# Kernel optimization log

Measured on AMD Instinct MI355X. Metric: run time of the kernel, lower is better.

The kernel has to match this reference:

```python
import jax, jax.numpy as jnp
import numpy as np

B, S, D, H, F, E = 4, 1024, 1024, 16, 4096, 8
HD = D // H  # head dim


def setup_inputs() -> dict:
    key = jax.random.key(0)
    ks = jax.random.split(key, 8)
    p = lambda k, shp: jax.random.normal(k, shp, jnp.float32) * 0.02
    return {
        "x": jax.random.normal(ks[0], (B, S, D), jnp.float32),
        "mask": jnp.ones((B, S), jnp.int32),
        "in_proj_w": p(ks[1], (3 * D, D)),
        "in_proj_b": jnp.zeros((3 * D,), jnp.float32),
        "out_proj_w": p(ks[2], (D, D)),
        "out_proj_b": jnp.zeros((D,), jnp.float32),
        "ln1_g": jnp.ones((D,), jnp.float32),
        "ln1_b": jnp.zeros((D,), jnp.float32),
        "ln2_g": jnp.ones((D,), jnp.float32),
        "ln2_b": jnp.zeros((D,), jnp.float32),
        "gate_w": p(ks[3], (E, D)),
        "gate_b": jnp.zeros((E,), jnp.float32),
        "w1": p(ks[4], (E, F, D)),
        "b1": jnp.zeros((E, F), jnp.float32),
        "w2": p(ks[5], (E, D, F)),
        "b2": jnp.zeros((E, D), jnp.float32),
    }


def _layernorm(x, g, b, eps=1e-5):
    m = x.mean(-1, keepdims=True)
    v = ((x - m) ** 2).mean(-1, keepdims=True)
    return (x - m) / jnp.sqrt(v + eps) * g + b


def _mha(x, key_pad, in_proj_w, in_proj_b, out_proj_w, out_proj_b):
    # combined QKV projection as in torch nn.MultiheadAttention
    qkv = x @ in_proj_w.T + in_proj_b  # (B,S,3D)
    q, k, v = jnp.split(qkv, 3, axis=-1)
    def heads(t):
        return t.reshape(B, S, H, HD).transpose(0, 2, 1, 3)  # (B,H,S,HD)
    q, k, v = heads(q), heads(k), heads(v)
    scores = jnp.einsum("bhqd,bhkd->bhqk", q, k) / jnp.sqrt(jnp.float32(HD))
    scores = jnp.where(key_pad[:, None, None, :], -1e30, scores)
    attn = jax.nn.softmax(scores, axis=-1)
    out = jnp.einsum("bhqk,bhkd->bhqd", attn, v)  # (B,H,S,HD)
    out = out.transpose(0, 2, 1, 3).reshape(B, S, D)
    return out @ out_proj_w.T + out_proj_b


def _moe(x, gate_w, gate_b, w1, b1, w2, b2):
    logits = x @ gate_w.T + gate_b            # (B,S,E)
    probs = jax.nn.softmax(logits, axis=-1)
    # dense all-expert FFN (faithful to original: every expert computed)
    h = jax.nn.relu(jnp.einsum("bsd,efd->bsef", x, w1) + b1)   # (B,S,E,F)
    all_out = jnp.einsum("bsef,edf->bsed", h, w2) + b2          # (B,S,E,D)
    top_vals, top_idx = jax.lax.top_k(probs, 2)                 # (B,S,2)
    weights = top_vals / (top_vals.sum(-1, keepdims=True) + 1e-9)
    sel = jnp.take_along_axis(all_out, top_idx[..., None], axis=2)  # (B,S,2,D)
    return (sel * weights[..., None]).sum(axis=2)


def reference(x, mask, in_proj_w, in_proj_b, out_proj_w, out_proj_b,
              ln1_g, ln1_b, ln2_g, ln2_b, gate_w, gate_b, w1, b1, w2, b2):
    key_pad = mask == 0  # (B,S) bool
    attn_out = _mha(x, key_pad, in_proj_w, in_proj_b, out_proj_w, out_proj_b)
    x1 = _layernorm(x + attn_out, ln1_g, ln1_b)
    ff = _moe(x1, gate_w, gate_b, w1, b1, w2, b2)
    return _layernorm(x1 + ff, ln2_g, ln2_b)
```

## Files before the change

### kernel.cpp

```cpp
#include <hip/hip_runtime.h>

typedef __attribute__((ext_vector_type(8))) short bf16x8;
typedef __attribute__((ext_vector_type(4))) float f32x4;

#define DEV __device__ __forceinline__

static constexpr int Bb = 4, Sq = 1024, Dd = 1024, Hh = 16, HDd = 64, Ff = 4096, Ee = 8;
static constexpr int Nn = Bb * Sq;
static constexpr int TD = 3 * Dd;
static constexpr int PMAX = 2 * Nn + Ee * 128;

DEV unsigned short f2bf(float x) {
  union { float f; unsigned u; } c; c.f = x;
  unsigned r = c.u + 0x7FFFu + ((c.u >> 16) & 1u);
  return (unsigned short)(r >> 16);
}

typedef const __attribute__((address_space(1))) unsigned int* gas_t;
typedef __attribute__((address_space(3))) unsigned int* las_t;
DEV void gload16(const void* g, void* l) {
  __builtin_amdgcn_global_load_lds((gas_t)g, (las_t)l, 16, 0, 0);
}

__global__ __launch_bounds__(256) void cvt_kernel(const float* __restrict__ in,
                                                  unsigned short* __restrict__ out) {
  int i = blockIdx.x * 256 + threadIdx.x;
  const float4 a = *(const float4*)(in + (size_t)i * 8);
  const float4 b = *(const float4*)(in + (size_t)i * 8 + 4);
  union { uint4 u; unsigned short s[8]; } pk;
  pk.s[0] = f2bf(a.x); pk.s[1] = f2bf(a.y); pk.s[2] = f2bf(a.z); pk.s[3] = f2bf(a.w);
  pk.s[4] = f2bf(b.x); pk.s[5] = f2bf(b.y); pk.s[6] = f2bf(b.z); pk.s[7] = f2bf(b.w);
  *(uint4*)(out + (size_t)i * 8) = pk.u;
}

template <int EPI>
__global__ __launch_bounds__(256) void gemm_bt(
    const unsigned short* __restrict__ A, const unsigned short* __restrict__ Bw,
    const float* __restrict__ bias, void* __restrict__ o0, void* __restrict__ o1,
    void* __restrict__ o2, int M, int Ncols, int K,
    const int* __restrict__ poff) {
  int bx, by;
  {
    const int gx = gridDim.x, nwg = gx * gridDim.y;
    int orig = blockIdx.y * gx + blockIdx.x;
    int q = nwg >> 3, r = nwg & 7;
    int xcd = orig & 7, lin = orig >> 3;
    int wg = (xcd < r ? xcd * (q + 1) : r * (q + 1) + (xcd - r) * q) + lin;
    bx = wg % gx; by = wg / gx;
  }
  const int m0 = bx * 128;
  int e = 0;
  if constexpr (EPI >= 2) {
    if (m0 >= poff[Ee]) return;
#pragma unroll
    for (int k = 1; k < Ee; ++k) if (m0 >= poff[k]) e = k;
  } else {
    if (m0 >= M) return;
  }
  const int n0 = by * 128;
  const unsigned short* Bptr = Bw + (size_t)e * Ncols * K;
  const float* biasptr = bias + e * Ncols;

  __shared__ __align__(128) unsigned short As[128 * 64];
  __shared__ __align__(128) unsigned short Bs[128 * 64];

  const int tid = threadIdx.x;
  const int lane = tid & 63, wid = tid >> 6;
  const int wm = wid >> 1, wn = wid & 1;
  const int lr = lane & 15, lk = lane >> 4;

  const char* aSrc[4]; const char* bSrc[4];
  char* aDst[4]; char* bDst[4];
#pragma unroll
  for (int it = 0; it < 4; ++it) {
    int b = it * 4096 + tid * 16;
    int r = b >> 7;
    int colb = (b & 127) ^ ((r & 7) << 4);
    aSrc[it] = (const char*)(A + (size_t)(m0 + r) * K) + colb;
    bSrc[it] = (const char*)(Bptr + (size_t)(n0 + r) * K) + colb;
    aDst[it] = (char*)As + it * 4096 + wid * 1024;
    bDst[it] = (char*)Bs + it * 4096 + wid * 1024;
  }
  int aOff[2][4], bOff[2][4];
#pragma unroll
  for (int ks = 0; ks < 2; ++ks)
#pragma unroll
    for (int i = 0; i < 4; ++i) {
      int ra = wm * 64 + i * 16 + lr;
      aOff[ks][i] = ra * 64 + (((ks * 4 + lk) ^ (ra & 7)) << 3);
      int rb = wn * 64 + i * 16 + lr;
      bOff[ks][i] = rb * 64 + (((ks * 4 + lk) ^ (rb & 7)) << 3);
    }

  f32x4 acc[4][4] = {};

  for (int k0 = 0; k0 < K; k0 += 64) {
#pragma unroll
    for (int it = 0; it < 4; ++it) gload16(aSrc[it] + (size_t)k0 * 2, aDst[it]);
#pragma unroll
    for (int it = 0; it < 4; ++it) gload16(bSrc[it] + (size_t)k0 * 2, bDst[it]);
    __syncthreads();
#pragma unroll
    for (int ks = 0; ks < 2; ++ks) {
      bf16x8 af[4], bfv[4];
#pragma unroll
      for (int mi = 0; mi < 4; ++mi) af[mi] = *(const bf16x8*)&As[aOff[ks][mi]];
#pragma unroll
      for (int ni = 0; ni < 4; ++ni) bfv[ni] = *(const bf16x8*)&Bs[bOff[ks][ni]];
#pragma unroll
      for (int mi = 0; mi < 4; ++mi)
#pragma unroll
        for (int ni = 0; ni < 4; ++ni)
          acc[mi][ni] = __builtin_amdgcn_mfma_f32_16x16x32_bf16(af[mi], bfv[ni], acc[mi][ni], 0, 0, 0);
    }
    __syncthreads();
  }

#pragma unroll
  for (int ni = 0; ni < 4; ++ni) {
    const int col = n0 + wn * 64 + ni * 16 + lr;
    const float bv = biasptr[col];
#pragma unroll
    for (int mi = 0; mi < 4; ++mi) {
#pragma unroll
      for (int i = 0; i < 4; ++i) {
        const int mloc = wm * 64 + mi * 16 + lk * 4 + i;
        float v = acc[mi][ni][i] + bv;
        if constexpr (EPI == 0) {
          int t = m0 + mloc;
          int which = col >> 10, jj = col & 1023, hh = jj >> 6, hd = jj & 63;
          int bb = t >> 10, s = t & 1023;
          unsigned short* dst = (which == 0) ? (unsigned short*)o0
                              : (which == 1) ? (unsigned short*)o1 : (unsigned short*)o2;
          dst[((size_t)(bb * Hh + hh) * Sq + s) * HDd + hd] = f2bf(v);
        } else if constexpr (EPI == 1) {
          ((float*)o0)[(size_t)(m0 + mloc) * Dd + col] = v;
        } else if constexpr (EPI == 2) {
          ((unsigned short*)o0)[(size_t)(m0 + mloc) * Ff + col] = f2bf(fmaxf(v, 0.f));
        } else {
          ((float*)o0)[(size_t)(m0 + mloc) * Dd + col] = v;
        }
      }
    }
  }
}

__global__ __launch_bounds__(256) void attn_kernel(
    const unsigned short* __restrict__ qb, const unsigned short* __restrict__ kb,
    const unsigned short* __restrict__ vb, const int* __restrict__ mask,
    unsigned short* __restrict__ attnb) {
  const int qt = blockIdx.x, h = blockIdx.y, b = blockIdx.z;
  const unsigned short* Q = qb + (size_t)(b * Hh + h) * Sq * HDd;
  const unsigned short* Kg = kb + (size_t)(b * Hh + h) * Sq * HDd;
  const unsigned short* Vg = vb + (size_t)(b * Hh + h) * Sq * HDd;

  __shared__ unsigned short Qs[64 * 72], Ks[64 * 72], Vt[64 * 72], Ps[64 * 72];
  __shared__ float Ssm[64 * 65];
  __shared__ float mS[64], lS[64], aS[64];
  __shared__ int mk[64];

  const int tid = threadIdx.x, lane = tid & 63, wid = tid >> 6;
  const int lr = lane & 15, lk = lane >> 4;

#pragma unroll
  for (int it = 0; it < 2; ++it) {
    int c = tid + it * 256; int r = c >> 3, kc = (c & 7) * 8;
    *(uint4*)&Qs[r * 72 + kc] = *(const uint4*)(Q + (size_t)(qt * 64 + r) * 64 + kc);
  }
  if (tid < 64) { mS[tid] = -1e30f; lS[tid] = 0.f; }

  f32x4 oacc[4] = {};

  for (int kt = 0; kt < 16; ++kt) {
    __syncthreads();
#pragma unroll
    for (int it = 0; it < 2; ++it) {
      int c = tid + it * 256; int r = c >> 3, kc = (c & 7) * 8;
      *(uint4*)&Ks[r * 72 + kc] = *(const uint4*)(Kg + (size_t)(kt * 64 + r) * 64 + kc);
    }
    {
      int kk = tid >> 2, hg = (tid & 3) * 16;
      union { uint4 u[2]; unsigned short s[16]; } tv;
      tv.u[0] = *(const uint4*)(Vg + (size_t)(kt * 64 + kk) * 64 + hg);
      tv.u[1] = *(const uint4*)(Vg + (size_t)(kt * 64 + kk) * 64 + hg + 8);
#pragma unroll
      for (int j = 0; j < 16; ++j) Vt[(hg + j) * 72 + kk] = tv.s[j];
    }
    if (tid < 64) mk[tid] = mask[b * Sq + kt * 64 + tid];
    __syncthreads();

    f32x4 sacc[4] = {};
#pragma unroll
    for (int ks = 0; ks < 2; ++ks) {
      bf16x8 aq = *(const bf16x8*)&Qs[(wid * 16 + lr) * 72 + ks * 32 + lk * 8];
#pragma unroll
      for (int ni = 0; ni < 4; ++ni) {
        bf16x8 bk = *(const bf16x8*)&Ks[(ni * 16 + lr) * 72 + ks * 32 + lk * 8];
        sacc[ni] = __builtin_amdgcn_mfma_f32_16x16x32_bf16(aq, bk, sacc[ni], 0, 0, 0);
      }
    }
#pragma unroll
    for (int ni = 0; ni < 4; ++ni)
#pragma unroll
      for (int i = 0; i < 4; ++i) {
        int r = wid * 16 + lk * 4 + i, cc = ni * 16 + lr;
        float v = sacc[ni][i] * 0.125f;
        if (mk[cc] == 0) v = -1e30f;
        Ssm[r * 65 + cc] = v;
      }
    __syncthreads();
    {
      int r = tid >> 2, cg = (tid & 3) * 16;
      float xv[16];
#pragma unroll
      for (int j = 0; j < 16; ++j) xv[j] = Ssm[r * 65 + cg + j];
      float mx = xv[0];
#pragma unroll
      for (int j = 1; j < 16; ++j) mx = fmaxf(mx, xv[j]);
      mx = fmaxf(mx, __shfl_xor(mx, 1));
      mx = fmaxf(mx, __shfl_xor(mx, 2));
      float mprev = mS[r];
      float mnew = fmaxf(mprev, mx);
      float sum = 0.f;
      union { uint4 u[2]; unsigned short s[16]; } pb;
#pragma unroll
      for (int j = 0; j < 16; ++j) {
        float pv = expf(xv[j] - mnew);
        sum += pv; pb.s[j] = f2bf(pv);
      }
      sum += __shfl_xor(sum, 1);
      sum += __shfl_xor(sum, 2);
      *(uint4*)&Ps[r * 72 + cg] = pb.u[0];
      *(uint4*)&Ps[r * 72 + cg + 8] = pb.u[1];
      if ((tid & 3) == 0) {
        float alpha = expf(mprev - mnew);
        mS[r] = mnew; aS[r] = alpha; lS[r] = lS[r] * alpha + sum;
      }
    }
    __syncthreads();
#pragma unroll
    for (int ni = 0; ni < 4; ++ni)
#pragma unroll
      for (int i = 0; i < 4; ++i)
        oacc[ni][i] *= aS[wid * 16 + lk * 4 + i];
#pragma unroll
    for (int ks = 0; ks < 2; ++ks) {
      bf16x8 ap = *(const bf16x8*)&Ps[(wid * 16 + lr) * 72 + ks * 32 + lk * 8];
#pragma unroll
      for (int ni = 0; ni < 4; ++ni) {
        bf16x8 bv = *(const bf16x8*)&Vt[(ni * 16 + lr) * 72 + ks * 32 + lk * 8];
        oacc[ni] = __builtin_amdgcn_mfma_f32_16x16x32_bf16(ap, bv, oacc[ni], 0, 0, 0);
      }
    }
  }
  __syncthreads();
#pragma unroll
  for (int ni = 0; ni < 4; ++ni)
#pragma unroll
    for (int i = 0; i < 4; ++i) {
      int r = wid * 16 + lk * 4 + i;
      int q = qt * 64 + r;
      float v = oacc[ni][i] / lS[r];
      attnb[((size_t)(b * Sq + q)) * Dd + h * 64 + ni * 16 + lr] = f2bf(v);
    }
}

__global__ __launch_bounds__(256) void ln_kernel(
    const float* __restrict__ a, const float* __restrict__ b2,
    const float* __restrict__ g, const float* __restrict__ beta,
    float* __restrict__ outf, unsigned short* __restrict__ outb) {
  const int t = blockIdx.x, tid = threadIdx.x;
  float4 v = *(const float4*)(a + (size_t)t * Dd + tid * 4);
  {
    float4 u = *(const float4*)(b2 + (size_t)t * Dd + tid * 4);
    v.x += u.x; v.y += u.y; v.z += u.z; v.w += u.w;
  }
  const int lane = tid & 63, wid = tid >> 6;
  float s = v.x + v.y + v.z + v.w;
  for (int sh = 1; sh < 64; sh <<= 1) s += __shfl_xor(s, sh);
  __shared__ float red[4], red2[4];
  if (lane == 0) red[wid] = s;
  __syncthreads();
  float mean = (red[0] + red[1] + red[2] + red[3]) * (1.f / Dd);
  float dx = v.x - mean, dy = v.y - mean, dz = v.z - mean, dw = v.w - mean;
  float q = dx * dx + dy * dy + dz * dz + dw * dw;
  for (int sh = 1; sh < 64; sh <<= 1) q += __shfl_xor(q, sh);
  if (lane == 0) red2[wid] = q;
  __syncthreads();
  float var = (red2[0] + red2[1] + red2[2] + red2[3]) * (1.f / Dd);
  float rstd = rsqrtf(var + 1e-5f);
  float4 gg = *(const float4*)(g + tid * 4);
  float4 bb = *(const float4*)(beta + tid * 4);
  float4 o;
  o.x = dx * rstd * gg.x + bb.x;
  o.y = dy * rstd * gg.y + bb.y;
  o.z = dz * rstd * gg.z + bb.z;
  o.w = dw * rstd * gg.w + bb.w;
  if (outf) *(float4*)(outf + (size_t)t * Dd + tid * 4) = o;
  if (outb) {
    ushort4 pk; pk.x = f2bf(o.x); pk.y = f2bf(o.y); pk.z = f2bf(o.z); pk.w = f2bf(o.w);
    *(ushort4*)(outb + (size_t)t * Dd + tid * 4) = pk;
  }
}

__global__ __launch_bounds__(256) void ln2_kernel(
    const float* __restrict__ x1f, const float* __restrict__ ffp,
    const int* __restrict__ inv, const float* __restrict__ wtok,
    const float* __restrict__ g, const float* __restrict__ beta,
    float* __restrict__ out) {
  const int t = blockIdx.x, tid = threadIdx.x;
  const int i0 = inv[2 * t], i1 = inv[2 * t + 1];
  const float w0 = wtok[2 * t], w1 = wtok[2 * t + 1];
  float4 v = *(const float4*)(x1f + (size_t)t * Dd + tid * 4);
  float4 u0 = *(const float4*)(ffp + (size_t)i0 * Dd + tid * 4);
  float4 u1 = *(const float4*)(ffp + (size_t)i1 * Dd + tid * 4);
  v.x += w0 * u0.x + w1 * u1.x; v.y += w0 * u0.y + w1 * u1.y;
  v.z += w0 * u0.z + w1 * u1.z; v.w += w0 * u0.w + w1 * u1.w;
  const int lane = tid & 63, wid = tid >> 6;
  float s = v.x + v.y + v.z + v.w;
  for (int sh = 1; sh < 64; sh <<= 1) s += __shfl_xor(s, sh);
  __shared__ float red[4], red2[4];
  if (lane == 0) red[wid] = s;
  __syncthreads();
  float mean = (red[0] + red[1] + red[2] + red[3]) * (1.f / Dd);
  float dx = v.x - mean, dy = v.y - mean, dz = v.z - mean, dw = v.w - mean;
  float q = dx * dx + dy * dy + dz * dz + dw * dw;
  for (int sh = 1; sh < 64; sh <<= 1) q += __shfl_xor(q, sh);
  if (lane == 0) red2[wid] = q;
  __syncthreads();
  float var = (red2[0] + red2[1] + red2[2] + red2[3]) * (1.f / Dd);
  float rstd = rsqrtf(var + 1e-5f);
  float4 gg = *(const float4*)(g + tid * 4);
  float4 bb = *(const float4*)(beta + tid * 4);
  float4 o;
  o.x = dx * rstd * gg.x + bb.x;
  o.y = dy * rstd * gg.y + bb.y;
  o.z = dz * rstd * gg.z + bb.z;
  o.w = dw * rstd * gg.w + bb.w;
  *(float4*)(out + (size_t)t * Dd + tid * 4) = o;
}

__global__ __launch_bounds__(256) void route_kernel(
    const float* __restrict__ x1f, const float* __restrict__ gw, const float* __restrict__ gb,
    int* __restrict__ cnt, int* __restrict__ tokslot, float* __restrict__ wtok) {
  __shared__ float gws[Ee * Dd];
  const int tid = threadIdx.x;
#pragma unroll
  for (int it = 0; it < 8; ++it) {
    int idx = (tid + it * 256) * 4;
    *(float4*)&gws[idx] = *(const float4*)(gw + idx);
  }
  __syncthreads();
  const int lane = tid & 63, wid = tid >> 6;
  for (int it = 0; it < 16; ++it) {
    int t = blockIdx.x * 64 + wid * 16 + it;
    float acc[Ee] = {};
    for (int i = 0; i < 16; ++i) {
      float xv = x1f[(size_t)t * Dd + i * 64 + lane];
#pragma unroll
      for (int e = 0; e < Ee; ++e) acc[e] += xv * gws[e * Dd + i * 64 + lane];
    }
#pragma unroll
    for (int e = 0; e < Ee; ++e) {
      float vv = acc[e];
      for (int sh = 1; sh < 64; sh <<= 1) vv += __shfl_xor(vv, sh);
      acc[e] = vv;
    }
    if (lane == 0) {
      float lg[Ee];
#pragma unroll
      for (int e = 0; e < Ee; ++e) lg[e] = acc[e] + gb[e];
      float m = lg[0];
#pragma unroll
      for (int e = 1; e < Ee; ++e) m = fmaxf(m, lg[e]);
      float p[Ee], ssum = 0.f;
#pragma unroll
      for (int e = 0; e < Ee; ++e) { p[e] = expf(lg[e] - m); ssum += p[e]; }
      int e0 = 0;
#pragma unroll
      for (int e = 1; e < Ee; ++e) if (p[e] > p[e0]) e0 = e;
      int e1 = -1;
#pragma unroll
      for (int e = 0; e < Ee; ++e) {
        if (e == e0) continue;
        if (e1 < 0 || p[e] > p[e1]) e1 = e;
      }
      float v0 = p[e0] / ssum, v1 = p[e1] / ssum;
      float wsum = v0 + v1 + 1e-9f;
      wtok[t * 2] = v0 / wsum; wtok[t * 2 + 1] = v1 / wsum;
      int p0 = atomicAdd(&cnt[e0], 1);
      tokslot[e0 * Nn + p0] = t * 2;
      int p1 = atomicAdd(&cnt[e1], 1);
      tokslot[e1 * Nn + p1] = t * 2 + 1;
    }
  }
}

__global__ void offsets_kernel(const int* __restrict__ cnt, int* __restrict__ poff) {
  if (threadIdx.x == 0) {
    int s = 0;
    for (int e = 0; e < Ee; ++e) { poff[e] = s; s += (cnt[e] + 127) & ~127; }
    poff[Ee] = s;
  }
}

__global__ __launch_bounds__(256) void pack_kernel(
    const unsigned short* __restrict__ x1b, const int* __restrict__ tokslot,
    const int* __restrict__ cnt, const int* __restrict__ poff,
    unsigned short* __restrict__ xg, int* __restrict__ inv) {
  const int tid = threadIdx.x;
  const int g = blockIdx.x * 8 + (tid >> 5);
  const int l = tid & 31;
  if (g >= poff[Ee]) return;
  int e = 0;
#pragma unroll
  for (int k = 1; k < Ee; ++k) if (g >= poff[k]) e = k;
  const int pos = g - poff[e];
  uint4* dst = (uint4*)(xg + (size_t)g * Dd);
  if (pos < cnt[e]) {
    const int ent = tokslot[e * Nn + pos];
    if (l == 0) inv[ent] = g;
    const uint4* src = (const uint4*)(x1b + (size_t)(ent >> 1) * Dd);
#pragma unroll
    for (int j = 0; j < 4; ++j) dst[l + j * 32] = src[l + j * 32];
  } else {
    const uint4 z = make_uint4(0, 0, 0, 0);
#pragma unroll
    for (int j = 0; j < 4; ++j) dst[l + j * 32] = z;
  }
}

extern "C" void kernel_launch(void* const* d_in, const int* in_sizes, int n_in,
                              void* d_out, int out_size, void* d_ws, size_t ws_size,
                              hipStream_t stream) {
  const float* x   = (const float*)d_in[0];
  const int*   msk = (const int*)d_in[1];
  const float* ipw = (const float*)d_in[2];
  const float* ipb = (const float*)d_in[3];
  const float* opw = (const float*)d_in[4];
  const float* opb = (const float*)d_in[5];
  const float* g1  = (const float*)d_in[6];
  const float* be1 = (const float*)d_in[7];
  const float* g2  = (const float*)d_in[8];
  const float* be2 = (const float*)d_in[9];
  const float* gw  = (const float*)d_in[10];
  const float* gb  = (const float*)d_in[11];
  const float* w1  = (const float*)d_in[12];
  const float* b1  = (const float*)d_in[13];
  const float* w2  = (const float*)d_in[14];
  const float* b2  = (const float*)d_in[15];
  float* out = (float*)d_out;

  char* p = (char*)d_ws;
  auto carve = [&](size_t bytes) { char* r = p; p += (bytes + 255) & ~(size_t)255; return r; };
  unsigned short* xb   = (unsigned short*)carve((size_t)Nn * Dd * 2);
  unsigned short* qb   = (unsigned short*)carve((size_t)Nn * Dd * 2);
  unsigned short* kb   = (unsigned short*)carve((size_t)Nn * Dd * 2);
  unsigned short* vb   = (unsigned short*)carve((size_t)Nn * Dd * 2);
  float* proj          = (float*)carve((size_t)Nn * Dd * 4);
  float* x1f           = (float*)carve((size_t)Nn * Dd * 4);
  unsigned short* x1b  = (unsigned short*)carve((size_t)Nn * Dd * 2);
  unsigned short* xg   = (unsigned short*)carve((size_t)PMAX * Dd * 2);
  float* ffp           = (float*)carve((size_t)PMAX * Dd * 4);
  unsigned short* hbuf = (unsigned short*)carve((size_t)PMAX * Ff * 2);
  unsigned short* wbuf = (unsigned short*)carve((size_t)Ee * Ff * Dd * 2);
  int* cnt             = (int*)carve(64);
  int* poff            = (int*)carve(64);
  int* tokslot         = (int*)carve((size_t)Ee * Nn * 4);
  float* wtok          = (float*)carve((size_t)2 * Nn * 4);
  int* inv             = (int*)carve((size_t)2 * Nn * 4);
  unsigned short* attnb = xb;

  cvt_kernel<<<Nn * Dd / 2048, 256, 0, stream>>>(x, xb);
  cvt_kernel<<<TD * Dd / 2048, 256, 0, stream>>>(ipw, wbuf);
  gemm_bt<0><<<dim3(Nn / 128, TD / 128), 256, 0, stream>>>(
      xb, wbuf, ipb, qb, kb, vb, Nn, TD, Dd, nullptr);
  attn_kernel<<<dim3(Sq / 64, Hh, Bb), 256, 0, stream>>>(qb, kb, vb, msk, attnb);
  cvt_kernel<<<Dd * Dd / 2048, 256, 0, stream>>>(opw, wbuf);
  gemm_bt<1><<<dim3(Nn / 128, Dd / 128), 256, 0, stream>>>(
      attnb, wbuf, opb, proj, nullptr, nullptr, Nn, Dd, Dd, nullptr);
  ln_kernel<<<Nn, 256, 0, stream>>>(x, proj, g1, be1, x1f, x1b);
  hipMemsetAsync(cnt, 0, 64, stream);
  route_kernel<<<Nn / 64, 256, 0, stream>>>(x1f, gw, gb, cnt, tokslot, wtok);
  offsets_kernel<<<1, 64, 0, stream>>>(cnt, poff);
  pack_kernel<<<PMAX / 8, 256, 0, stream>>>(x1b, tokslot, cnt, poff, xg, inv);
  cvt_kernel<<<Ee * Ff * Dd / 2048, 256, 0, stream>>>(w1, wbuf);
  gemm_bt<2><<<dim3(PMAX / 128, Ff / 128), 256, 0, stream>>>(
      xg, wbuf, b1, hbuf, nullptr, nullptr, PMAX, Ff, Dd, poff);
  cvt_kernel<<<Ee * Dd * Ff / 2048, 256, 0, stream>>>(w2, wbuf);
  gemm_bt<3><<<dim3(PMAX / 128, Dd / 128), 256, 0, stream>>>(
      hbuf, wbuf, b2, ffp, nullptr, nullptr, PMAX, Dd, Ff, poff);
  ln2_kernel<<<Nn, 256, 0, stream>>>(x1f, ffp, inv, wtok, g2, be2, out);
}
```

Measured before the change: 683.7 us.

## Triple-buffer GEMM LDS tiles with K=32 steps and async prefetch

Replaces the single-buffered 64-wide K loop, which had two barriers per step, with a three-stage ring of 32-wide K tiles. Loads for step t+2 are issued while step t computes, using an explicit vmcnt wait and one barrier per iteration. The LDS swizzle is redone for the 64-byte rows. The goal is to hide global-load latency behind MFMA work. In exchange it doubles the number of loop iterations and barriers, and the hand-tuned vmcnt count must match the four loads issued per stage.

Result: faster. 627.5 us (-8.2%).

```diff
diff --git a/kernel.cpp b/kernel.cpp
--- a/kernel.cpp
+++ b/kernel.cpp
@@ -61,59 +61,70 @@
   const unsigned short* Bptr = Bw + (size_t)e * Ncols * K;
   const float* biasptr = bias + e * Ncols;
 
-  __shared__ __align__(128) unsigned short As[128 * 64];
-  __shared__ __align__(128) unsigned short Bs[128 * 64];
+  __shared__ __align__(128) unsigned short As[3 * 128 * 32];
+  __shared__ __align__(128) unsigned short Bs[3 * 128 * 32];
 
   const int tid = threadIdx.x;
   const int lane = tid & 63, wid = tid >> 6;
   const int wm = wid >> 1, wn = wid & 1;
   const int lr = lane & 15, lk = lane >> 4;
 
-  const char* aSrc[4]; const char* bSrc[4];
-  char* aDst[4]; char* bDst[4];
-#pragma unroll
-  for (int it = 0; it < 4; ++it) {
+  const char* aSrc[2]; const char* bSrc[2];
+  int dOff[2];
+#pragma unroll
+  for (int it = 0; it < 2; ++it) {
     int b = it * 4096 + tid * 16;
-    int r = b >> 7;
-    int colb = (b & 127) ^ ((r & 7) << 4);
+    int r = b >> 6;
+    int colb = (b & 63) ^ (((r >> 1) & 3) << 4);
     aSrc[it] = (const char*)(A + (size_t)(m0 + r) * K) + colb;
     bSrc[it] = (const char*)(Bptr + (size_t)(n0 + r) * K) + colb;
-    aDst[it] = (char*)As + it * 4096 + wid * 1024;
-    bDst[it] = (char*)Bs + it * 4096 + wid * 1024;
-  }
-  int aOff[2][4], bOff[2][4];
-#pragma unroll
-  for (int ks = 0; ks < 2; ++ks)
-#pragma unroll
-    for (int i = 0; i < 4; ++i) {
-      int ra = wm * 64 + i * 16 + lr;
-      aOff[ks][i] = ra * 64 + (((ks * 4 + lk) ^ (ra & 7)) << 3);
-      int rb = wn * 64 + i * 16 + lr;
-      bOff[ks][i] = rb * 64 + (((ks * 4 + lk) ^ (rb & 7)) << 3);
-    }
+    dOff[it] = it * 4096 + wid * 1024;
+  }
+  int aOff[4], bOff[4];
+#pragma unroll
+  for (int i = 0; i < 4; ++i) {
+    int ra = wm * 64 + i * 16 + lr;
+    aOff[i] = ra * 32 + ((lk ^ ((ra >> 1) & 3)) << 3);
+    int rb = wn * 64 + i * 16 + lr;
+    bOff[i] = rb * 32 + ((lk ^ ((rb >> 1) & 3)) << 3);
+  }
+
+  auto STAGE = [&](int t, int buf) {
+#pragma unroll
+    for (int it = 0; it < 2; ++it) {
+      gload16(aSrc[it] + (size_t)t * 64, (char*)As + buf * 8192 + dOff[it]);
+      gload16(bSrc[it] + (size_t)t * 64, (char*)Bs + buf * 8192 + dOff[it]);
+    }
+  };
 
   f32x4 acc[4][4] = {};
-
-  for (int k0 = 0; k0 < K; k0 += 64) {
-#pragma unroll
-    for (int it = 0; it < 4; ++it) gload16(aSrc[it] + (size_t)k0 * 2, aDst[it]);
-#pragma unroll
-    for (int it = 0; it < 4; ++it) gload16(bSrc[it] + (size_t)k0 * 2, bDst[it]);
-    __syncthreads();
-#pragma unroll
-    for (int ks = 0; ks < 2; ++ks) {
-      bf16x8 af[4], bfv[4];
-#pragma unroll
-      for (int mi = 0; mi < 4; ++mi) af[mi] = *(const bf16x8*)&As[aOff[ks][mi]];
-#pragma unroll
-      for (int ni = 0; ni < 4; ++ni) bfv[ni] = *(const bf16x8*)&Bs[bOff[ks][ni]];
-#pragma unroll
-      for (int mi = 0; mi < 4; ++mi)
-#pragma unroll
-        for (int ni = 0; ni < 4; ++ni)
-          acc[mi][ni] = __builtin_amdgcn_mfma_f32_16x16x32_bf16(af[mi], bfv[ni], acc[mi][ni], 0, 0, 0);
-    }
-    __syncthreads();
+  const int NT = K >> 5;
+
+  STAGE(0, 0);
+  STAGE(1, 1);
+  int cb = 0;
+  int sb = 2;
+  for (int t = 0; t < NT; ++t) {
+    if (t + 1 < NT) asm volatile("s_waitcnt vmcnt(4)" ::: "memory");
+    else            asm volatile("s_waitcnt vmcnt(0)" ::: "memory");
+    __builtin_amdgcn_sched_barrier(0);
+    __builtin_amdgcn_s_barrier();
+    __builtin_amdgcn_sched_barrier(0);
+    if (t + 2 < NT) STAGE(t + 2, sb);
+    const unsigned short* Ab = As + cb * 4096;
+    const unsigned short* Bb2 = Bs + cb * 4096;
+    bf16x8 af[4], bfv[4];
+#pragma unroll
+    for (int mi = 0; mi < 4; ++mi) af[mi] = *(const bf16x8*)&Ab[aOff[mi]];
+#pragma unroll
+    for (int ni = 0; ni < 4; ++ni) bfv[ni] = *(const bf16x8*)&Bb2[bOff[ni]];
+#pragma unroll
+    for (int mi = 0; mi < 4; ++mi)
+#pragma unroll
+      for (int ni = 0; ni < 4; ++ni)
+        acc[mi][ni] = __builtin_amdgcn_mfma_f32_16x16x32_bf16(af[mi], bfv[ni], acc[mi][ni], 0, 0, 0);
+    cb = (cb == 2) ? 0 : cb + 1;
+    sb = (sb == 2) ? 0 : sb + 1;
   }
 
 #pragma unroll
```
